# Performance work log

Measured on AMD Instinct MI355X. Metric: run time of the kernel, lower is better.

Reference implementation:

```python
import jax, jax.numpy as jnp
import numpy as np

D = 768        # d_model
F = 8192       # dict_size
N_UP = 3       # number of upstream autoencoders
K = 64         # topk
B, S = 2, 1024


def setup_inputs() -> dict:
    key = jax.random.key(0)
    ks = jax.random.split(key, 10)
    sc = 1.0 / np.sqrt(D)
    return {
        "feature_buffer": jnp.zeros((B, S, F), jnp.float32),
        "x": jax.random.normal(ks[0], (B, S, D), jnp.float32),
        "up_feats": jax.random.uniform(ks[1], (N_UP, B, S, F), jnp.float32),
        "W_enc": jax.random.normal(ks[2], (D, F), jnp.float32) * sc,
        "b_enc": jax.random.normal(ks[3], (F,), jnp.float32) * 0.01,
        "W_dec": jax.random.normal(ks[4], (F, D), jnp.float32) * sc,
        "b_dec": jax.random.normal(ks[5], (D,), jnp.float32) * 0.01,
        "up_W_dec": jax.random.normal(ks[6], (N_UP, F, D), jnp.float32) * sc,
        "up_b_dec": jax.random.normal(ks[7], (N_UP, D), jnp.float32) * 0.01,
        "conn_mask": jax.random.randint(ks[8], (N_UP, F, F), 0, 2).astype(bool),
        "k": K,
    }


def reference(feature_buffer, x, up_feats, W_enc, b_enc, W_dec, b_dec,
              up_W_dec, up_b_dec, conn_mask, k):
    # initial contribs: residual stream through current encoder
    approx = jnp.einsum("bsd,df->bsf", x, W_enc)            # [B,S,F]
    upstream_bias = jnp.zeros((D,), x.dtype)
    # accumulate pruned contributions from each upstream AE
    for i in range(up_feats.shape[0]):
        upstream_bias = upstream_bias + up_b_dec[i]
        # virtual weights up_dict -> down_dict, pruned by connection mask
        virt = (up_W_dec[i] @ W_enc) * conn_mask[i].astype(x.dtype)  # [F_up,F_down]
        approx = approx + jnp.einsum("bsf,fg->bsg", up_feats[i], virt)
    # bias correction: upstream decoder biases through encoder, plus encoder bias
    approx = approx + upstream_bias @ W_enc + b_enc          # [B,S,F]
    # topk + relu + scatter into the feature buffer
    top_vals, top_idx = jax.lax.top_k(approx, k)             # [B,S,k]
    top_vals = jax.nn.relu(top_vals)
    flat = feature_buffer.reshape(-1, F)
    rows = jnp.arange(flat.shape[0])[:, None]
    feat = flat.at[rows, top_idx.reshape(-1, k)].set(top_vals.reshape(-1, k))
    feat = feat.reshape(feature_buffer.shape)
    # decode
    return jnp.einsum("bsf,fd->bsd", feat, W_dec) + b_dec
```

## Files before the change

kernel.cpp:

```cpp
#include <hip/hip_runtime.h>
#include <hip/hip_bf16.h>


#define D_DIM 768
#define F_DIM 8192

typedef _Float16 f16;
typedef _Float16 f16x8 __attribute__((ext_vector_type(8)));
typedef float f32x4 __attribute__((ext_vector_type(4)));

#define BMN 128
#define BUFB 32768
#define PLNB 16384

__device__ inline void split_f32(float v, f16& h, f16& l) {
    float hf = (float)(f16)v;
    if (__builtin_fabsf(hf) < 6.1035156e-5f) hf = 0.f;
    h = (f16)hf;
    l = (f16)((v - hf) * 2048.0f);
}

template<int MODE>
__global__ __launch_bounds__(256, 2)
void mfma_gemm(const f16* __restrict__ Ap,
               const f16* __restrict__ Bp,
               float* __restrict__ C, int ldc,
               f16* __restrict__ Vp,
               const float* __restrict__ bias,
               const unsigned char* __restrict__ conn, int upIdx,
               const int* __restrict__ flagp,
               int K, int fdBase)
{
    __shared__ char lds[2 * BUFB];
    const int tid = threadIdx.x;
    const int bm = blockIdx.y * BMN;
    const int bn = blockIdx.x * BMN;
    const int w  = tid >> 6;
    const int l  = tid & 63;
    const int wr = (w >> 1) * 64;
    const int wc = (w & 1) * 64;

    const char* gsrc[8];
    #pragma unroll
    for (int j = 0; j < 8; ++j) {
        const int c = tid + 256 * j;
        const int p = c >> 10;
        const int q = c & 1023;
        const int r = q >> 3;
        const int sp = q & 7;
        const int slog = sp ^ (r & 7);
        const f16* base = p ? Bp : Ap;
        const int row0 = p ? bn : bm;
        gsrc[j] = (const char*)base + (size_t)(row0 + r) * ((size_t)K * 4)
                  + slog * 16;
    }

    #define STAGE(BUFSEL)                                                     \
        _Pragma("unroll")                                                     \
        for (int j = 0; j < 8; ++j) {                                         \
            __builtin_amdgcn_global_load_lds(                                 \
                (const __attribute__((address_space(1))) void*)gsrc[j],       \
                (__attribute__((address_space(3))) void*)                     \
                    (lds + (BUFSEL) * BUFB + (tid + 256 * j) * 16),           \
                16, 0, 0);                                                    \
            gsrc[j] += 128;                       \
        }

    f32x4 accH[4][4], accM[4][4];
    const f32x4 zero = {0.f, 0.f, 0.f, 0.f};
    #pragma unroll
    for (int a = 0; a < 4; ++a)
        #pragma unroll
        for (int b = 0; b < 4; ++b) { accH[a][b] = zero; accM[a][b] = zero; }

    const int steps = K >> 5;
    const int fr = l & 15;
    const int ks = l >> 4;

    int offAH[4], offBH[4], offAL[4], offBL[4];
    #pragma unroll
    for (int f = 0; f < 4; ++f) {
        const int ra = wr + f * 16 + fr;
        const int rb = wc + f * 16 + fr;
        offAH[f] = ra * 128 + ((ks ^ (ra & 7)) * 16);
        offAL[f] = ra * 128 + (((4 + ks) ^ (ra & 7)) * 16);
        offBH[f] = PLNB + rb * 128 + ((ks ^ (rb & 7)) * 16);
        offBL[f] = PLNB + rb * 128 + (((4 + ks) ^ (rb & 7)) * 16);
    }

    STAGE(0);
    int cur = 0;
    for (int t = 0; t < steps; ++t) {
        asm volatile("s_waitcnt vmcnt(0)" ::: "memory");
        __syncthreads();

        const char* Lb = lds + cur * BUFB;
        f16x8 ah[4], bh[4];
        #pragma unroll
        for (int mf = 0; mf < 4; ++mf) ah[mf] = *(const f16x8*)(Lb + offAH[mf]);
        #pragma unroll
        for (int nf = 0; nf < 4; ++nf) bh[nf] = *(const f16x8*)(Lb + offBH[nf]);

        if (t + 1 < steps) STAGE(cur ^ 1);

        f16x8 al[4], bl[4];
        #pragma unroll
        for (int nf = 0; nf < 4; ++nf) bl[nf] = *(const f16x8*)(Lb + offBL[nf]);
        #pragma unroll
        for (int mf = 0; mf < 4; ++mf) al[mf] = *(const f16x8*)(Lb + offAL[mf]);

        __builtin_amdgcn_s_setprio(1);
        #pragma unroll
        for (int nf = 0; nf < 4; ++nf)
            #pragma unroll
            for (int mf = 0; mf < 4; ++mf)
                accH[mf][nf] = __builtin_amdgcn_mfma_f32_16x16x32_f16(
                    ah[mf], bh[nf], accH[mf][nf], 0, 0, 0);
        __builtin_amdgcn_s_setprio(0);

        __builtin_amdgcn_s_setprio(1);
        #pragma unroll
        for (int nf = 0; nf < 4; ++nf)
            #pragma unroll
            for (int mf = 0; mf < 4; ++mf)
                accM[mf][nf] = __builtin_amdgcn_mfma_f32_16x16x32_f16(
                    ah[mf], bl[nf], accM[mf][nf], 0, 0, 0);
        #pragma unroll
        for (int mf = 0; mf < 4; ++mf)
            #pragma unroll
            for (int nf = 0; nf < 4; ++nf)
                accM[mf][nf] = __builtin_amdgcn_mfma_f32_16x16x32_f16(
                    al[mf], bh[nf], accM[mf][nf], 0, 0, 0);
        __builtin_amdgcn_s_setprio(0);

        cur ^= 1;
    }
    #undef STAGE

    const float MS = 4.8828125e-4f;
    const int flag = (MODE == 1) ? *flagp : 0;

    #pragma unroll
    for (int mf = 0; mf < 4; ++mf) {
        const int row0 = wr + mf * 16 + (l >> 4) * 4;
        #pragma unroll
        for (int nf = 0; nf < 4; ++nf) {
            const int col = wc + nf * 16 + (l & 15);
            float v[4];
            #pragma unroll
            for (int rr = 0; rr < 4; ++rr)
                v[rr] = accH[mf][nf][rr] + accM[mf][nf][rr] * MS;

            if (MODE == 0) {
                const float bb = bias[bn + col];
                #pragma unroll
                for (int rr = 0; rr < 4; ++rr)
                    C[(size_t)(bm + row0 + rr) * ldc + (bn + col)] = v[rr] + bb;
            } else if (MODE == 2) {
                #pragma unroll
                for (int rr = 0; rr < 4; ++rr) {
                    float* cp = &C[(size_t)(bm + row0 + rr) * ldc + (bn + col)];
                    *cp = *cp + v[rr];
                }
            } else {
                const size_t fu = (size_t)(bn + col);
                const size_t fd0 = (size_t)(fdBase + bm + row0);
                int m[4];
                if (flag == 1) {
                    const int4 mm = *(const int4*)((const int*)conn +
                        (size_t)upIdx * F_DIM * F_DIM + fu * F_DIM + fd0);
                    m[0] = mm.x; m[1] = mm.y; m[2] = mm.z; m[3] = mm.w;
                } else if (flag == 0) {
                    const uchar4 mm = *(const uchar4*)(conn +
                        (size_t)upIdx * F_DIM * F_DIM + fu * F_DIM + fd0);
                    m[0] = mm.x; m[1] = mm.y; m[2] = mm.z; m[3] = mm.w;
                } else if (flag == 2) {
                    const long long* pp = (const long long*)conn +
                        (size_t)upIdx * F_DIM * F_DIM + fu * F_DIM + fd0;
                    m[0] = (int)pp[0]; m[1] = (int)pp[1];
                    m[2] = (int)pp[2]; m[3] = (int)pp[3];
                } else {
                    const float4 mm = *(const float4*)((const float*)conn +
                        (size_t)upIdx * F_DIM * F_DIM + fu * F_DIM + fd0);
                    m[0] = mm.x != 0.f; m[1] = mm.y != 0.f;
                    m[2] = mm.z != 0.f; m[3] = mm.w != 0.f;
                }
                const size_t kblk = (fu >> 5) * 64 + (fu & 31);
                #pragma unroll
                for (int rr = 0; rr < 4; ++rr) {
                    const float vv = m[rr] ? v[rr] : 0.f;
                    f16 hh, ll;
                    split_f32(vv, hh, ll);
                    const size_t o = (size_t)(bm + row0 + rr) * (2 * F_DIM) + kblk;
                    Vp[o] = hh; Vp[o + 32] = ll;
                }
            }
        }
    }
}

__global__ __launch_bounds__(256)
void split_kernel(const float* __restrict__ src, f16* __restrict__ dst,
                  size_t n, int K)
{
    const size_t e = ((size_t)blockIdx.x * 256 + threadIdx.x) * 8;
    if (e >= n) return;
    const size_t r = e / (size_t)K;
    const int k = (int)(e - r * (size_t)K);
    const float4 a = *(const float4*)(src + e);
    const float4 b = *(const float4*)(src + e + 4);
    f16 hv[8], lv[8];
    const float s[8] = {a.x, a.y, a.z, a.w, b.x, b.y, b.z, b.w};
    #pragma unroll
    for (int i = 0; i < 8; ++i) split_f32(s[i], hv[i], lv[i]);
    const size_t base = r * (size_t)(2 * K) + (size_t)((k >> 5) * 64 + (k & 31));
    *(f16x8*)(dst + base)      = *(const f16x8*)hv;
    *(f16x8*)(dst + base + 32) = *(const f16x8*)lv;
}

__global__ __launch_bounds__(256)
void transpose_split_kernel(const float* __restrict__ W, f16* __restrict__ dst)
{
    const int f = blockIdx.x * 256 + threadIdx.x;
    for (int dc = 0; dc < D_DIM / 8; ++dc) {
        const int k = dc * 8;
        f16 hv[8], lv[8];
        #pragma unroll
        for (int j = 0; j < 8; ++j)
            split_f32(W[(size_t)(k + j) * F_DIM + f], hv[j], lv[j]);
        const size_t base = (size_t)f * (2 * D_DIM) + (k >> 5) * 64 + (k & 31);
        *(f16x8*)(dst + base)      = *(const f16x8*)hv;
        *(f16x8*)(dst + base + 32) = *(const f16x8*)lv;
    }
}

__global__ void detect_kernel(const int* __restrict__ conn, int* __restrict__ flag)
{
    __shared__ int not01, notf01, odd_nz;
    if (threadIdx.x == 0) { not01 = 0; notf01 = 0; odd_nz = 0; }
    __syncthreads();
    const int4 v = ((const int4*)conn)[threadIdx.x];
    const unsigned a[4] = {(unsigned)v.x, (unsigned)v.y,
                           (unsigned)v.z, (unsigned)v.w};
    int l_not01 = 0, l_notf = 0;
    #pragma unroll
    for (int i = 0; i < 4; ++i) {
        if (a[i] > 1u) l_not01 = 1;
        if (a[i] != 0u && a[i] != 0x3F800000u) l_notf = 1;
    }
    if (l_not01) atomicOr(&not01, 1);
    if (l_notf)  atomicOr(&notf01, 1);
    if (a[1] | a[3]) atomicOr(&odd_nz, 1);
    __syncthreads();
    if (threadIdx.x == 0) {
        int f;
        if (!not01)        f = odd_nz ? 1 : 2;
        else if (!notf01)  f = 3;
        else               f = 0;
        *flag = f;
    }
}

__global__ void bias2_kernel(const float* __restrict__ W_enc,
                             const float* __restrict__ b_enc,
                             const float* __restrict__ up_b_dec,
                             int nup, float* __restrict__ bias2)
{
    const int g = blockIdx.x * 256 + threadIdx.x;
    if (g >= F_DIM) return;
    float s = b_enc[g];
    for (int d = 0; d < D_DIM; ++d) {
        float ub = 0.f;
        for (int i = 0; i < nup; ++i) ub += up_b_dec[i * D_DIM + d];
        s = __builtin_fmaf(ub, W_enc[(size_t)d * F_DIM + g], s);
    }
    bias2[g] = s;
}

__global__ __launch_bounds__(256)
void topk_decode_kernel(const float* __restrict__ approx,
                        const float* __restrict__ W_dec,
                        const float* __restrict__ b_dec,
                        const int* __restrict__ kptr,
                        float* __restrict__ out)
{
    __shared__ unsigned keys[F_DIM];
    __shared__ int hist[256];
    __shared__ unsigned sh_prefix;
    __shared__ int sh_need;
    __shared__ int sel_cnt, eq_cnt;
    __shared__ int sidx[128];
    __shared__ float sval[128];
    __shared__ int eqidx[1024];

    const int tid = threadIdx.x;
    const int row = blockIdx.x;
    const int k = *kptr;
    const float* arow = approx + (size_t)row * F_DIM;

    for (int j = tid; j < F_DIM; j += 256) {
        unsigned u = __float_as_uint(arow[j]);
        u = (u & 0x80000000u) ? ~u : (u | 0x80000000u);
        keys[j] = u;
    }
    if (tid == 0) { sh_prefix = 0u; sh_need = k; sel_cnt = 0; eq_cnt = 0; }
    __syncthreads();

    for (int shift = 24; shift >= 0; shift -= 8) {
        if (tid < 256) hist[tid] = 0;
        __syncthreads();
        const unsigned pfx = sh_prefix;
        for (int j = tid; j < F_DIM; j += 256) {
            const unsigned u = keys[j];
            const bool match =
                (shift == 24) || ((u >> (shift + 8)) == (pfx >> (shift + 8)));
            if (match) atomicAdd(&hist[(u >> shift) & 255], 1);
        }
        __syncthreads();
        if (tid == 0) {
            int need = sh_need;
            for (int b = 255; b >= 0; --b) {
                const int c = hist[b];
                if (c >= need) {
                    sh_prefix = pfx | ((unsigned)b << shift);
                    sh_need = need;
                    break;
                }
                need -= c;
            }
        }
        __syncthreads();
    }
    const unsigned T = sh_prefix;
    const int r = sh_need;

    for (int j = tid; j < F_DIM; j += 256) {
        const unsigned u = keys[j];
        if (u > T) {
            const int p = atomicAdd(&sel_cnt, 1);
            sidx[p] = j;
        } else if (u == T) {
            const int p = atomicAdd(&eq_cnt, 1);
            if (p < 1024) eqidx[p] = j;
        }
    }
    __syncthreads();

    if (tid == 0) {
        const int m = sel_cnt;
        const int e = eq_cnt < 1024 ? eq_cnt : 1024;
        for (int t2 = 0; t2 < r; ++t2) {
            int best = 0x7FFFFFFF, bi = -1;
            for (int q = 0; q < e; ++q) {
                const int v = eqidx[q];
                if (v >= 0 && v < best) { best = v; bi = q; }
            }
            if (bi >= 0) { eqidx[bi] = -1; sidx[m + t2] = best; }
        }
        sel_cnt = m + r;
        const int n = sel_cnt;
        for (int a2 = 1; a2 < n; ++a2) {
            const int v = sidx[a2];
            int b2 = a2 - 1;
            while (b2 >= 0 && sidx[b2] > v) { sidx[b2 + 1] = sidx[b2]; --b2; }
            sidx[b2 + 1] = v;
        }
    }
    __syncthreads();

    const int total = sel_cnt;
    for (int j = tid; j < total; j += 256) {
        const float v = arow[sidx[j]];
        sval[j] = v > 0.f ? v : 0.f;
    }
    __syncthreads();

    float acc0 = b_dec[tid];
    float acc1 = b_dec[tid + 256];
    float acc2 = b_dec[tid + 512];
    for (int j = 0; j < total; ++j) {
        const float v = sval[j];
        const float* wv = W_dec + (size_t)sidx[j] * D_DIM;
        acc0 = __builtin_fmaf(v, wv[tid],       acc0);
        acc1 = __builtin_fmaf(v, wv[tid + 256], acc1);
        acc2 = __builtin_fmaf(v, wv[tid + 512], acc2);
    }
    float* orow = out + (size_t)row * D_DIM;
    orow[tid] = acc0;
    orow[tid + 256] = acc1;
    orow[tid + 512] = acc2;
}

extern "C" void kernel_launch(void* const* d_in, const int* in_sizes, int n_in,
                              void* d_out, int out_size, void* d_ws, size_t ws_size,
                              hipStream_t stream)
{
    const float* x         = (const float*)d_in[1];
    const float* up_feats  = (const float*)d_in[2];
    const float* W_enc     = (const float*)d_in[3];
    const float* b_enc     = (const float*)d_in[4];
    const float* W_dec     = (const float*)d_in[5];
    const float* b_dec     = (const float*)d_in[6];
    const float* up_W_dec  = (const float*)d_in[7];
    const float* up_b_dec  = (const float*)d_in[8];
    const unsigned char* conn = (const unsigned char*)d_in[9];
    const int* kptr        = (const int*)d_in[10];

    const int BS  = in_sizes[1] / D_DIM;
    const int NUP = in_sizes[8] / D_DIM;

    char* ws = (char*)d_ws;
    size_t off = 0;
    auto alloc = [&](size_t bytes) -> char* {
        off = (off + 255) & ~(size_t)255;
        char* p = ws + off; off += bytes; return p;
    };
    float* approx = (float*)alloc((size_t)BS * F_DIM * 4);
    float* bias2  = (float*)alloc(F_DIM * 4);
    int*   flag   = (int*)alloc(256);
    f16* xp   = (f16*)alloc((size_t)BS * D_DIM * 4);
    f16* Wtp  = (f16*)alloc((size_t)F_DIM * D_DIM * 4);
    f16* uwdp = (f16*)alloc((size_t)NUP * F_DIM * D_DIM * 4);
    f16* ufp  = (f16*)alloc((size_t)NUP * BS * F_DIM * 4);

    off = (off + 255) & ~(size_t)255;
    const size_t rem = (ws_size > off) ? ws_size - off : 0;
    int FC = (int)((rem / ((size_t)F_DIM * 4)) / 128 * 128);
    if (FC > F_DIM) FC = F_DIM;
    if (FC < 128) FC = 128;
    f16* vp = (f16*)alloc((size_t)FC * F_DIM * 4);

    detect_kernel<<<1, 256, 0, stream>>>((const int*)conn, flag);
    bias2_kernel<<<F_DIM / 256, 256, 0, stream>>>(W_enc, b_enc, up_b_dec, NUP, bias2);

    split_kernel<<<(unsigned)((size_t)BS * D_DIM / 2048), 256, 0, stream>>>(
        x, xp, (size_t)BS * D_DIM, D_DIM);
    split_kernel<<<(unsigned)((size_t)NUP * F_DIM * D_DIM / 2048), 256, 0, stream>>>(
        up_W_dec, uwdp, (size_t)NUP * F_DIM * D_DIM, D_DIM);
    split_kernel<<<(unsigned)((size_t)NUP * BS * F_DIM / 2048), 256, 0, stream>>>(
        up_feats, ufp, (size_t)NUP * BS * F_DIM, F_DIM);
    transpose_split_kernel<<<F_DIM / 256, 256, 0, stream>>>(W_enc, Wtp);

    mfma_gemm<0><<<dim3(F_DIM / BMN, BS / BMN), 256, 0, stream>>>(
        xp, Wtp, approx, F_DIM, nullptr, bias2,
        nullptr, 0, flag, D_DIM, 0);

    for (int i = 0; i < NUP; ++i) {
        for (int fc = 0; fc < F_DIM; fc += FC) {
            const int chunk = (F_DIM - fc) < FC ? (F_DIM - fc) : FC;
            mfma_gemm<1><<<dim3(F_DIM / BMN, chunk / BMN), 256, 0, stream>>>(
                Wtp + (size_t)fc * (2 * D_DIM),
                uwdp + (size_t)i * F_DIM * (2 * D_DIM),
                nullptr, 0, vp, nullptr,
                conn, i, flag, D_DIM, fc);
            mfma_gemm<2><<<dim3(chunk / BMN, BS / BMN), 256, 0, stream>>>(
                ufp + (size_t)i * BS * (2 * F_DIM),
                vp,
                approx + fc, F_DIM, nullptr, nullptr,
                nullptr, 0, flag, F_DIM, 0);
        }
    }

    topk_decode_kernel<<<BS, 256, 0, stream>>>(
        approx, W_dec, b_dec, kptr, (float*)d_out);
}
```

Measured before the change: 3.786 ms.

## Switch GEMM to 32x32x16 MFMA, XCD-aware block remap, cap chunk size

Replaces the 16x16x32 MFMA tiling with 32x32x16 MFMA instructions, using 2x2 fragments per wave with 16-wide accumulators, and rewrites the LDS fragment offsets and epilogue indexing to match. It also remaps block IDs so consecutive tiles land on the same XCD, which should improve L2 reuse. The virtual-weight chunk size is capped at 4096 rows, halving from there until it fits the workspace. The larger MFMA is meant to cut LDS reads and instruction count per flop, but the different accumulator layout makes the epilogue's strided writes less coalesced, and the remap assumes the block count is divisible by 8.

```diff
diff --git a/kernel.cpp b/kernel.cpp
--- a/kernel.cpp
+++ b/kernel.cpp
@@ -7,7 +7,7 @@
 
 typedef _Float16 f16;
 typedef _Float16 f16x8 __attribute__((ext_vector_type(8)));
-typedef float f32x4 __attribute__((ext_vector_type(4)));
+typedef float f32x16 __attribute__((ext_vector_type(16)));
 
 #define BMN 128
 #define BUFB 32768
@@ -33,12 +33,21 @@
 {
     __shared__ char lds[2 * BUFB];
     const int tid = threadIdx.x;
-    const int bm = blockIdx.y * BMN;
-    const int bn = blockIdx.x * BMN;
+
+    const unsigned gx = gridDim.x;
+    const unsigned nwg = gx * gridDim.y;
+    const unsigned bid0 = blockIdx.y * gx + blockIdx.x;
+    const unsigned cpx = nwg >> 3;
+    const unsigned bid = (bid0 & 7u) * cpx + (bid0 >> 3);
+    const int bm = (int)(bid / gx) * BMN;
+    const int bn = (int)(bid % gx) * BMN;
+
     const int w  = tid >> 6;
     const int l  = tid & 63;
     const int wr = (w >> 1) * 64;
     const int wc = (w & 1) * 64;
+    const int ln = l & 31;
+    const int ls = l >> 5;
 
     const char* gsrc[8];
     #pragma unroll
@@ -66,27 +75,29 @@
             gsrc[j] += 128;                       \
         }
 
-    f32x4 accH[4][4], accM[4][4];
-    const f32x4 zero = {0.f, 0.f, 0.f, 0.f};
-    #pragma unroll
-    for (int a = 0; a < 4; ++a)
-        #pragma unroll
-        for (int b = 0; b < 4; ++b) { accH[a][b] = zero; accM[a][b] = zero; }
+    f32x16 accH[2][2], accM[2][2];
+    #pragma unroll
+    for (int a = 0; a < 2; ++a)
+        #pragma unroll
+        for (int b = 0; b < 2; ++b) {
+            accH[a][b] = (f32x16)(0.f);
+            accM[a][b] = (f32x16)(0.f);
+        }
 
     const int steps = K >> 5;
-    const int fr = l & 15;
-    const int ks = l >> 4;
-
-    int offAH[4], offBH[4], offAL[4], offBL[4];
-    #pragma unroll
-    for (int f = 0; f < 4; ++f) {
-        const int ra = wr + f * 16 + fr;
-        const int rb = wc + f * 16 + fr;
-        offAH[f] = ra * 128 + ((ks ^ (ra & 7)) * 16);
-        offAL[f] = ra * 128 + (((4 + ks) ^ (ra & 7)) * 16);
-        offBH[f] = PLNB + rb * 128 + ((ks ^ (rb & 7)) * 16);
-        offBL[f] = PLNB + rb * 128 + (((4 + ks) ^ (rb & 7)) * 16);
-    }
+
+    int offAH[2][2], offAL[2][2], offBH[2][2], offBL[2][2];
+    #pragma unroll
+    for (int f = 0; f < 2; ++f)
+        #pragma unroll
+        for (int kh = 0; kh < 2; ++kh) {
+            const int ra = wr + f * 32 + ln;
+            const int rb = wc + f * 32 + ln;
+            offAH[f][kh] = ra * 128 + (((kh * 2 + ls) ^ (ra & 7)) * 16);
+            offAL[f][kh] = ra * 128 + (((4 + kh * 2 + ls) ^ (ra & 7)) * 16);
+            offBH[f][kh] = PLNB + rb * 128 + (((kh * 2 + ls) ^ (rb & 7)) * 16);
+            offBL[f][kh] = PLNB + rb * 128 + (((4 + kh * 2 + ls) ^ (rb & 7)) * 16);
+        }
 
     STAGE(0);
     int cur = 0;
@@ -95,42 +106,54 @@
         __syncthreads();
 
         const char* Lb = lds + cur * BUFB;
-        f16x8 ah[4], bh[4];
-        #pragma unroll
-        for (int mf = 0; mf < 4; ++mf) ah[mf] = *(const f16x8*)(Lb + offAH[mf]);
-        #pragma unroll
-        for (int nf = 0; nf < 4; ++nf) bh[nf] = *(const f16x8*)(Lb + offBH[nf]);
+        f16x8 ah[2][2], bh[2][2];
+        #pragma unroll
+        for (int f = 0; f < 2; ++f)
+            #pragma unroll
+            for (int kh = 0; kh < 2; ++kh) {
+                ah[f][kh] = *(const f16x8*)(Lb + offAH[f][kh]);
+                bh[f][kh] = *(const f16x8*)(Lb + offBH[f][kh]);
+            }
 
         if (t + 1 < steps) STAGE(cur ^ 1);
 
-        f16x8 al[4], bl[4];
-        #pragma unroll
-        for (int nf = 0; nf < 4; ++nf) bl[nf] = *(const f16x8*)(Lb + offBL[nf]);
-        #pragma unroll
-        for (int mf = 0; mf < 4; ++mf) al[mf] = *(const f16x8*)(Lb + offAL[mf]);
+        f16x8 al[2][2], bl[2][2];
+        #pragma unroll
+        for (int f = 0; f < 2; ++f)
+            #pragma unroll
+            for (int kh = 0; kh < 2; ++kh) {
+                bl[f][kh] = *(const f16x8*)(Lb + offBL[f][kh]);
+                al[f][kh] = *(const f16x8*)(Lb + offAL[f][kh]);
+            }
 
         __builtin_amdgcn_s_setprio(1);
         #pragma unroll
-        for (int nf = 0; nf < 4; ++nf)
-            #pragma unroll
-            for (int mf = 0; mf < 4; ++mf)
-                accH[mf][nf] = __builtin_amdgcn_mfma_f32_16x16x32_f16(
-                    ah[mf], bh[nf], accH[mf][nf], 0, 0, 0);
+        for (int kh = 0; kh < 2; ++kh)
+            #pragma unroll
+            for (int nf = 0; nf < 2; ++nf)
+                #pragma unroll
+                for (int mf = 0; mf < 2; ++mf)
+                    accH[mf][nf] = __builtin_amdgcn_mfma_f32_32x32x16_f16(
+                        ah[mf][kh], bh[nf][kh], accH[mf][nf], 0, 0, 0);
         __builtin_amdgcn_s_setprio(0);
 
         __builtin_amdgcn_s_setprio(1);
         #pragma unroll
-        for (int nf = 0; nf < 4; ++nf)
-            #pragma unroll
-            for (int mf = 0; mf < 4; ++mf)
-                accM[mf][nf] = __builtin_amdgcn_mfma_f32_16x16x32_f16(
-                    ah[mf], bl[nf], accM[mf][nf], 0, 0, 0);
-        #pragma unroll
-        for (int mf = 0; mf < 4; ++mf)
-            #pragma unroll
-            for (int nf = 0; nf < 4; ++nf)
-                accM[mf][nf] = __builtin_amdgcn_mfma_f32_16x16x32_f16(
-                    al[mf], bh[nf], accM[mf][nf], 0, 0, 0);
+        for (int kh = 0; kh < 2; ++kh)
+            #pragma unroll
+            for (int nf = 0; nf < 2; ++nf)
+                #pragma unroll
+                for (int mf = 0; mf < 2; ++mf)
+                    accM[mf][nf] = __builtin_amdgcn_mfma_f32_32x32x16_f16(
+                        ah[mf][kh], bl[nf][kh], accM[mf][nf], 0, 0, 0);
+        #pragma unroll
+        for (int kh = 0; kh < 2; ++kh)
+            #pragma unroll
+            for (int mf = 0; mf < 2; ++mf)
+                #pragma unroll
+                for (int nf = 0; nf < 2; ++nf)
+                    accM[mf][nf] = __builtin_amdgcn_mfma_f32_32x32x16_f16(
+                        al[mf][kh], bh[nf][kh], accM[mf][nf], 0, 0, 0);
         __builtin_amdgcn_s_setprio(0);
 
         cur ^= 1;
@@ -141,58 +164,63 @@
     const int flag = (MODE == 1) ? *flagp : 0;
 
     #pragma unroll
-    for (int mf = 0; mf < 4; ++mf) {
-        const int row0 = wr + mf * 16 + (l >> 4) * 4;
-        #pragma unroll
-        for (int nf = 0; nf < 4; ++nf) {
-            const int col = wc + nf * 16 + (l & 15);
-            float v[4];
-            #pragma unroll
-            for (int rr = 0; rr < 4; ++rr)
-                v[rr] = accH[mf][nf][rr] + accM[mf][nf][rr] * MS;
-
-            if (MODE == 0) {
-                const float bb = bias[bn + col];
+    for (int mf = 0; mf < 2; ++mf) {
+        #pragma unroll
+        for (int nf = 0; nf < 2; ++nf) {
+            const int gcol = bn + wc + nf * 32 + ln;
+            #pragma unroll
+            for (int g = 0; g < 4; ++g) {
+                const int row0 = wr + mf * 32 + g * 8 + 4 * ls;
+                float v[4];
                 #pragma unroll
                 for (int rr = 0; rr < 4; ++rr)
-                    C[(size_t)(bm + row0 + rr) * ldc + (bn + col)] = v[rr] + bb;
-            } else if (MODE == 2) {
-                #pragma unroll
-                for (int rr = 0; rr < 4; ++rr) {
-                    float* cp = &C[(size_t)(bm + row0 + rr) * ldc + (bn + col)];
-                    *cp = *cp + v[rr];
-                }
-            } else {
-                const size_t fu = (size_t)(bn + col);
-                const size_t fd0 = (size_t)(fdBase + bm + row0);
-                int m[4];
-                if (flag == 1) {
-                    const int4 mm = *(const int4*)((const int*)conn +
-                        (size_t)upIdx * F_DIM * F_DIM + fu * F_DIM + fd0);
-                    m[0] = mm.x; m[1] = mm.y; m[2] = mm.z; m[3] = mm.w;
-                } else if (flag == 0) {
-                    const uchar4 mm = *(const uchar4*)(conn +
-                        (size_t)upIdx * F_DIM * F_DIM + fu * F_DIM + fd0);
-                    m[0] = mm.x; m[1] = mm.y; m[2] = mm.z; m[3] = mm.w;
-                } else if (flag == 2) {
-                    const long long* pp = (const long long*)conn +
-                        (size_t)upIdx * F_DIM * F_DIM + fu * F_DIM + fd0;
-                    m[0] = (int)pp[0]; m[1] = (int)pp[1];
-                    m[2] = (int)pp[2]; m[3] = (int)pp[3];
+                    v[rr] = accH[mf][nf][g * 4 + rr]
+                          + accM[mf][nf][g * 4 + rr] * MS;
+
+                if (MODE == 0) {
+                    const float bb = bias[gcol];
+                    #pragma unroll
+                    for (int rr = 0; rr < 4; ++rr)
+                        C[(size_t)(bm + row0 + rr) * ldc + gcol] = v[rr] + bb;
+                } else if (MODE == 2) {
+                    #pragma unroll
+                    for (int rr = 0; rr < 4; ++rr) {
+                        float* cp = &C[(size_t)(bm + row0 + rr) * ldc + gcol];
+                        *cp = *cp + v[rr];
+                    }
                 } else {
-                    const float4 mm = *(const float4*)((const float*)conn +
-                        (size_t)upIdx * F_DIM * F_DIM + fu * F_DIM + fd0);
-                    m[0] = mm.x != 0.f; m[1] = mm.y != 0.f;
-                    m[2] = mm.z != 0.f; m[3] = mm.w != 0.f;
-                }
-                const size_t kblk = (fu >> 5) * 64 + (fu & 31);
-                #pragma unroll
-                for (int rr = 0; rr < 4; ++rr) {
-                    const float vv = m[rr] ? v[rr] : 0.f;
-                    f16 hh, ll;
-                    split_f32(vv, hh, ll);
-                    const size_t o = (size_t)(bm + row0 + rr) * (2 * F_DIM) + kblk;
-                    Vp[o] = hh; Vp[o + 32] = ll;
+                    const size_t fu = (size_t)gcol;
+                    const size_t fd0 = (size_t)(fdBase + bm + row0);
+                    int m[4];
+                    if (flag == 1) {
+                        const int4 mm = *(const int4*)((const int*)conn +
+                            (size_t)upIdx * F_DIM * F_DIM + fu * F_DIM + fd0);
+                        m[0] = mm.x; m[1] = mm.y; m[2] = mm.z; m[3] = mm.w;
+                    } else if (flag == 0) {
+                        const uchar4 mm = *(const uchar4*)(conn +
+                            (size_t)upIdx * F_DIM * F_DIM + fu * F_DIM + fd0);
+                        m[0] = mm.x; m[1] = mm.y; m[2] = mm.z; m[3] = mm.w;
+                    } else if (flag == 2) {
+                        const long long* pp = (const long long*)conn +
+                            (size_t)upIdx * F_DIM * F_DIM + fu * F_DIM + fd0;
+                        m[0] = (int)pp[0]; m[1] = (int)pp[1];
+                        m[2] = (int)pp[2]; m[3] = (int)pp[3];
+                    } else {
+                        const float4 mm = *(const float4*)((const float*)conn +
+                            (size_t)upIdx * F_DIM * F_DIM + fu * F_DIM + fd0);
+                        m[0] = mm.x != 0.f; m[1] = mm.y != 0.f;
+                        m[2] = mm.z != 0.f; m[3] = mm.w != 0.f;
+                    }
+                    const size_t kblk = (fu >> 5) * 64 + (fu & 31);
+                    #pragma unroll
+                    for (int rr = 0; rr < 4; ++rr) {
+                        const float vv = m[rr] ? v[rr] : 0.f;
+                        f16 hh, ll;
+                        split_f32(vv, hh, ll);
+                        const size_t o =
+                            (size_t)(bm + row0 + rr) * (2 * F_DIM) + kblk;
+                        Vp[o] = hh; Vp[o + 32] = ll;
+                    }
                 }
             }
         }
@@ -425,9 +453,8 @@
 
     off = (off + 255) & ~(size_t)255;
     const size_t rem = (ws_size > off) ? ws_size - off : 0;
-    int FC = (int)((rem / ((size_t)F_DIM * 4)) / 128 * 128);
-    if (FC > F_DIM) FC = F_DIM;
-    if (FC < 128) FC = 128;
+    int FC = 4096;
+    while (FC > 128 && (size_t)FC * F_DIM * 4 > rem) FC >>= 1;
     f16* vp = (f16*)alloc((size_t)FC * F_DIM * 4);
 
     detect_kernel<<<1, 256, 0, stream>>>((const int*)conn, flag);
```

Measured after the change: 4.657 ms. +23.0%, slower.
